# Optimization experiments

Hardware: AMD Instinct MI355X
Metric: run time of the kernel (lower is better)

The kernel has to match this reference:

```python
import jax, jax.numpy as jnp
import numpy as np

EMBED_DIM = 256
NUM_HEADS = 8
HEAD_WIDTH = 32
B, L = 2, 2048


def setup_inputs() -> dict:
    key = jax.random.key(0)
    k1, k2, k3, k4 = jax.random.split(key, 4)
    x = jax.random.normal(k1, (B, L, EMBED_DIM), dtype=jnp.float32)
    bias = jax.random.normal(k2, (B, L, L, NUM_HEADS), dtype=jnp.float32)
    # torch Linear weights: [out_features, in_features]
    W_proj = jax.random.normal(k3, (3 * EMBED_DIM, EMBED_DIM), dtype=jnp.float32) * (EMBED_DIM ** -0.5)
    W_o = jax.random.normal(k4, (EMBED_DIM, EMBED_DIM), dtype=jnp.float32) * (EMBED_DIM ** -0.5)
    b_o = jnp.zeros((EMBED_DIM,), dtype=jnp.float32)
    return {"x": x, "bias": bias, "W_proj": W_proj, "W_o": W_o, "b_o": b_o}


def reference(x, bias, W_proj, W_o, b_o):
    b, l, _ = x.shape
    h, hw = NUM_HEADS, HEAD_WIDTH
    # fused QKV projection: (b, l, 3*E)
    t = jnp.einsum('ble,fe->blf', x, W_proj)
    # rearrange '... l (h c) -> ... h l c' with c = 3*hw, then split
    t = t.reshape(b, l, h, 3 * hw).transpose(0, 2, 1, 3)  # (b, h, l, 3*hw)
    q, k, v = jnp.split(t, 3, axis=-1)
    q = q * (hw ** -0.5)
    a = jnp.einsum('bhqc,bhkc->bhqk', q, k)
    a = a + bias.transpose(0, 3, 1, 2)  # (b, h, lq, lk)
    a = jax.nn.softmax(a, axis=-1)
    y = jnp.einsum('bhqk,bhkc->bqhc', a, v)
    y = y.reshape(b, l, h * hw)
    return jnp.einsum('ble,fe->blf', y, W_o) + b_o
```

## Files before the change

### kernel.cpp

```cpp
#include <hip/hip_runtime.h>
#include <math.h>

#define NH   8
#define HW   32
#define LSEQ 2048
#define EMB  256
#define BB   2

typedef short bf16x8 __attribute__((ext_vector_type(8)));
typedef float f32x4  __attribute__((ext_vector_type(4)));
typedef unsigned short u16x4 __attribute__((ext_vector_type(4)));

__device__ __forceinline__ unsigned short f2bf(float x) {
  union { float f; unsigned u; } v; v.f = x;
  unsigned r = v.u + 0x7fffu + ((v.u >> 16) & 1u);
  return (unsigned short)(r >> 16);
}
__device__ __forceinline__ float bf2f(unsigned short h) {
  union { float f; unsigned u; } v; v.u = ((unsigned)h) << 16;
  return v.f;
}
__device__ __forceinline__ void split2(float x, unsigned short& h, unsigned short& l) {
  h = f2bf(x);
  l = f2bf(x - bf2f(h));
}

__global__ __launch_bounds__(256) void presplit(
    const float* __restrict__ X, const float* __restrict__ Wp,
    const float* __restrict__ Wo,
    unsigned short* __restrict__ Xh, unsigned short* __restrict__ Xl,
    unsigned short* __restrict__ Wph, unsigned short* __restrict__ Wpl,
    unsigned short* __restrict__ Woh, unsigned short* __restrict__ Wol) {
  const int NX = 4096 * 256, NP = 768 * 256, NO = 256 * 256;
  const int total4 = (NX + NP + NO) >> 2;
  int i4 = blockIdx.x * 256 + threadIdx.x;
  if (i4 >= total4) return;
  int e = i4 << 2;
  const float* src;
  unsigned short *dh, *dl;
  int off;
  if (e < NX)           { src = X;  dh = Xh;  dl = Xl;  off = e; }
  else if (e < NX + NP) { src = Wp; dh = Wph; dl = Wpl; off = e - NX; }
  else                  { src = Wo; dh = Woh; dl = Wol; off = e - NX - NP; }
  float4 v = *(const float4*)(src + off);
  u16x4 h, l;
  unsigned short hh, ll;
  split2(v.x, hh, ll); h[0] = hh; l[0] = ll;
  split2(v.y, hh, ll); h[1] = hh; l[1] = ll;
  split2(v.z, hh, ll); h[2] = hh; l[2] = ll;
  split2(v.w, hh, ll); h[3] = hh; l[3] = ll;
  *(u16x4*)(dh + off) = h;
  *(u16x4*)(dl + off) = l;
}

__global__ __launch_bounds__(256, 4) void qkv_gemm(
    const unsigned short* __restrict__ Xh, const unsigned short* __restrict__ Xl,
    const unsigned short* __restrict__ Wph, const unsigned short* __restrict__ Wpl,
    unsigned short* __restrict__ Qh, unsigned short* __restrict__ Ql,
    unsigned short* __restrict__ Kh, unsigned short* __restrict__ Kl,
    unsigned short* __restrict__ Vth, unsigned short* __restrict__ Vtl) {
  const int t = threadIdx.x;
  const int w = t >> 6, lane = t & 63;
  const int col = lane & 15, quad = lane >> 4;
  const int m0 = blockIdx.y * 64 + w * 16;
  const int n0 = blockIdx.x * 64;
  const size_t xoff = (size_t)(m0 + col) * 256 + quad * 8;

  f32x4 acc[4];
#pragma unroll
  for (int nt = 0; nt < 4; ++nt) acc[nt] = (f32x4){0.f, 0.f, 0.f, 0.f};

#pragma unroll
  for (int es = 0; es < 8; ++es) {
    bf16x8 ah = *(const bf16x8*)(Xh + xoff + es * 32);
    bf16x8 al = *(const bf16x8*)(Xl + xoff + es * 32);
#pragma unroll
    for (int nt = 0; nt < 4; ++nt) {
      const size_t woff = (size_t)(n0 + nt * 16 + col) * 256 + es * 32 + quad * 8;
      bf16x8 bh = *(const bf16x8*)(Wph + woff);
      bf16x8 bl = *(const bf16x8*)(Wpl + woff);
      acc[nt] = __builtin_amdgcn_mfma_f32_16x16x32_bf16(ah, bh, acc[nt], 0, 0, 0);
      acc[nt] = __builtin_amdgcn_mfma_f32_16x16x32_bf16(ah, bl, acc[nt], 0, 0, 0);
      acc[nt] = __builtin_amdgcn_mfma_f32_16x16x32_bf16(al, bh, acc[nt], 0, 0, 0);
    }
  }

  const float qscale = 0.17677669529663687f;
#pragma unroll
  for (int nt = 0; nt < 4; ++nt) {
    const int f = n0 + nt * 16 + col;
    const int hd = f / 96, r0 = f - hd * 96;
#pragma unroll
    for (int r = 0; r < 4; ++r) {
      const int m = m0 + quad * 4 + r;
      const int bbv = m >> 11, ll = m & 2047;
      float v = acc[nt][r];
      unsigned short hi, lo;
      if (r0 < 64) {
        float sv = (r0 < 32) ? v * qscale : v;
        split2(sv, hi, lo);
        size_t idx = ((size_t)(bbv * NH + hd) * LSEQ + ll) * HW + (r0 & 31);
        if (r0 < 32) { Qh[idx] = hi; Ql[idx] = lo; }
        else         { Kh[idx] = hi; Kl[idx] = lo; }
      } else {
        split2(v, hi, lo);
        size_t idx = ((size_t)(bbv * NH + hd) * HW + (r0 - 64)) * LSEQ + ll;
        Vth[idx] = hi; Vtl[idx] = lo;
      }
    }
  }
}

__global__ __launch_bounds__(512, 4) void attn(
    const unsigned short* __restrict__ Qh, const unsigned short* __restrict__ Ql,
    const unsigned short* __restrict__ Kh, const unsigned short* __restrict__ Kl,
    const unsigned short* __restrict__ Vth, const unsigned short* __restrict__ Vtl,
    const float* __restrict__ Bias, float* __restrict__ Yp,
    float* __restrict__ Mm, float* __restrict__ Ll) {
  __shared__ __attribute__((aligned(16))) float Bst[4 * 32 * 72];
  __shared__ __attribute__((aligned(16))) unsigned Pbuf[8 * 1152];
  const int t = threadIdx.x;
  const int w = t >> 6, lane = t & 63;
  const int col = lane & 15, quad = lane >> 4;
  const int head = w >> 1, wks = w & 1;
  const int x = blockIdx.x;
  const int p = ((x >> 4) << 3) | (x & 7);
  const int hh = (x >> 3) & 1;
  const int ks = p & 1;
  const int b = (p >> 1) & 1;
  const int q0g = (p >> 2) * 32;
  const int hg = hh * 4 + head;
  const int kbase = ks * 1024;

  const size_t bhoff = (size_t)(b * NH + hg) * LSEQ * HW;
  const unsigned short* Qhp = Qh + bhoff;
  const unsigned short* Qlp = Ql + bhoff;
  const unsigned short* Khp = Kh + bhoff;
  const unsigned short* Klp = Kl + bhoff;
  const unsigned short* Vhp = Vth + bhoff;
  const unsigned short* Vlp = Vtl + bhoff;
  unsigned* Pw = &Pbuf[w * 1152];

  bf16x8 Qbh[2], Qbl[2];
#pragma unroll
  for (int qt = 0; qt < 2; ++qt) {
    size_t off = (size_t)(q0g + qt * 16 + col) * HW + quad * 8;
    Qbh[qt] = *(const bf16x8*)(Qhp + off);
    Qbl[qt] = *(const bf16x8*)(Qlp + off);
  }

  f32x4 o[2][2];
#pragma unroll
  for (int ct = 0; ct < 2; ++ct)
#pragma unroll
    for (int qt = 0; qt < 2; ++qt) o[ct][qt] = (f32x4){0.f, 0.f, 0.f, 0.f};
  float m_i[2] = {-1e30f, -1e30f}, l_i[2] = {0.f, 0.f};

  const int sq = w, sk = lane;
  float4 bsr[4];
#pragma unroll
  for (int u = 0; u < 4; ++u)
    bsr[u] = *(const float4*)&Bias[(((size_t)(b * LSEQ + q0g + u * 8 + sq)) * LSEQ +
                                    kbase + sk) * NH + hh * 4];

#pragma unroll 1
  for (int it = 0; it < 16; ++it) {
    __syncthreads();
    const int kw = kbase + it * 64 + wks * 32;
    bf16x8 Kah[2], Kal[2], Vah[2], Val[2];
#pragma unroll
    for (int kt = 0; kt < 2; ++kt) {
      size_t off = (size_t)(kw + kt * 16 + col) * HW + quad * 8;
      Kah[kt] = *(const bf16x8*)(Khp + off);
      Kal[kt] = *(const bf16x8*)(Klp + off);
    }
#pragma unroll
    for (int ct = 0; ct < 2; ++ct) {
      size_t off = (size_t)(ct * 16 + col) * LSEQ + kw + quad * 8;
      Vah[ct] = *(const bf16x8*)(Vhp + off);
      Val[ct] = *(const bf16x8*)(Vlp + off);
    }
#pragma unroll
    for (int u = 0; u < 4; ++u) {
      const int qq = u * 8 + sq;
      Bst[0 * 2304 + qq * 72 + sk] = bsr[u].x;
      Bst[1 * 2304 + qq * 72 + sk] = bsr[u].y;
      Bst[2 * 2304 + qq * 72 + sk] = bsr[u].z;
      Bst[3 * 2304 + qq * 72 + sk] = bsr[u].w;
    }
    if (it < 15) {
#pragma unroll
      for (int u = 0; u < 4; ++u)
        bsr[u] = *(const float4*)&Bias[(((size_t)(b * LSEQ + q0g + u * 8 + sq)) * LSEQ +
                                        kbase + (it + 1) * 64 + sk) * NH + hh * 4];
    }
    __syncthreads();

    f32x4 s[2][2];
#pragma unroll
    for (int kt = 0; kt < 2; ++kt)
#pragma unroll
      for (int qt = 0; qt < 2; ++qt) {
        f32x4 a = *(const f32x4*)&Bst[head * 2304 + (qt * 16 + col) * 72 +
                                      wks * 32 + kt * 16 + quad * 4];
        a = __builtin_amdgcn_mfma_f32_16x16x32_bf16(Kah[kt], Qbh[qt], a, 0, 0, 0);
        a = __builtin_amdgcn_mfma_f32_16x16x32_bf16(Kah[kt], Qbl[qt], a, 0, 0, 0);
        a = __builtin_amdgcn_mfma_f32_16x16x32_bf16(Kal[kt], Qbh[qt], a, 0, 0, 0);
        s[kt][qt] = a;
      }

    float alpha[2];
#pragma unroll
    for (int qt = 0; qt < 2; ++qt) {
      float mx = s[0][qt][0];
#pragma unroll
      for (int r = 1; r < 4; ++r) mx = fmaxf(mx, s[0][qt][r]);
#pragma unroll
      for (int r = 0; r < 4; ++r) mx = fmaxf(mx, s[1][qt][r]);
      mx = fmaxf(mx, __shfl_xor(mx, 16, 64));
      mx = fmaxf(mx, __shfl_xor(mx, 32, 64));
      float mnew = fmaxf(m_i[qt], mx);
      float al = __expf(m_i[qt] - mnew);
      float ps = 0.f;
#pragma unroll
      for (int kt = 0; kt < 2; ++kt)
#pragma unroll
        for (int r = 0; r < 4; ++r) {
          float pv = __expf(s[kt][qt][r] - mnew);
          s[kt][qt][r] = pv;
          ps += pv;
        }
      ps += __shfl_xor(ps, 16, 64);
      ps += __shfl_xor(ps, 32, 64);
      l_i[qt] = l_i[qt] * al + ps;
      m_i[qt] = mnew;
      alpha[qt] = al;
#pragma unroll
      for (int ct = 0; ct < 2; ++ct)
#pragma unroll
        for (int r = 0; r < 4; ++r) o[ct][qt][r] *= al;
    }

#pragma unroll
    for (int kt = 0; kt < 2; ++kt)
#pragma unroll
      for (int qt = 0; qt < 2; ++qt)
#pragma unroll
        for (int r = 0; r < 4; ++r) {
          unsigned short hi, lo; split2(s[kt][qt][r], hi, lo);
          Pw[(kt * 16 + quad * 4 + r) * 34 + qt * 16 + col] =
              (unsigned)hi | ((unsigned)lo << 16);
        }
    bf16x8 Pbh[2], Pbl[2];
#pragma unroll
    for (int qt = 0; qt < 2; ++qt) {
#pragma unroll
      for (int j = 0; j < 8; ++j) {
        unsigned d = Pw[(quad * 8 + j) * 34 + qt * 16 + col];
        Pbh[qt][j] = (short)(d & 0xffffu);
        Pbl[qt][j] = (short)(d >> 16);
      }
    }
#pragma unroll
    for (int ct = 0; ct < 2; ++ct)
#pragma unroll
      for (int qt = 0; qt < 2; ++qt) {
        f32x4 a = o[ct][qt];
        a = __builtin_amdgcn_mfma_f32_16x16x32_bf16(Vah[ct], Pbh[qt], a, 0, 0, 0);
        a = __builtin_amdgcn_mfma_f32_16x16x32_bf16(Vah[ct], Pbl[qt], a, 0, 0, 0);
        a = __builtin_amdgcn_mfma_f32_16x16x32_bf16(Val[ct], Pbh[qt], a, 0, 0, 0);
        o[ct][qt] = a;
      }
  }

  __syncthreads();
  float* Pwf = (float*)Pw;
  if (wks == 1) {
#pragma unroll
    for (int ct = 0; ct < 2; ++ct)
#pragma unroll
      for (int qt = 0; qt < 2; ++qt)
#pragma unroll
        for (int r = 0; r < 4; ++r)
          Pwf[(ct * 16 + quad * 4 + r) * 34 + qt * 16 + col] = o[ct][qt][r];
    if (quad == 0) {
#pragma unroll
      for (int qt = 0; qt < 2; ++qt) {
        Pwf[1088 + qt * 16 + col] = m_i[qt];
        Pwf[1120 + qt * 16 + col] = l_i[qt];
      }
    }
  }
  __syncthreads();
  if (wks == 0) {
    const float* Pp = Pwf + 1152;
#pragma unroll
    for (int qt = 0; qt < 2; ++qt) {
      float m2 = Pp[1088 + qt * 16 + col];
      float l2 = Pp[1120 + qt * 16 + col];
      float mm = fmaxf(m_i[qt], m2);
      float a1 = __expf(m_i[qt] - mm);
      float a2 = __expf(m2 - mm);
      float lm = l_i[qt] * a1 + l2 * a2;
      const size_t row = (size_t)ks * 4096 + b * LSEQ + q0g + qt * 16 + col;
      if (quad == 0) {
        Mm[row * 8 + hg] = mm;
        Ll[row * 8 + hg] = lm;
      }
#pragma unroll
      for (int ct = 0; ct < 2; ++ct) {
        float4 res;
        res.x = o[ct][qt][0] * a1 + Pp[(ct * 16 + quad * 4 + 0) * 34 + qt * 16 + col] * a2;
        res.y = o[ct][qt][1] * a1 + Pp[(ct * 16 + quad * 4 + 1) * 34 + qt * 16 + col] * a2;
        res.z = o[ct][qt][2] * a1 + Pp[(ct * 16 + quad * 4 + 2) * 34 + qt * 16 + col] * a2;
        res.w = o[ct][qt][3] * a1 + Pp[(ct * 16 + quad * 4 + 3) * 34 + qt * 16 + col] * a2;
        *(float4*)&Yp[row * EMB + hg * HW + ct * 16 + quad * 4] = res;
      }
    }
  }
}

__global__ __launch_bounds__(256, 4) void out_gemm(
    const float* __restrict__ Yp, const float* __restrict__ Mm,
    const float* __restrict__ Ll, const unsigned short* __restrict__ Woh,
    const unsigned short* __restrict__ Wol, const float* __restrict__ bo,
    float* __restrict__ Out) {
  const int t = threadIdx.x;
  const int w = t >> 6, lane = t & 63;
  const int col = lane & 15, quad = lane >> 4;
  const int m0 = blockIdx.y * 64 + w * 16;
  const int n0 = blockIdx.x * 64;
  const int grow = m0 + col;
  const float* o1p = Yp + (size_t)grow * 256 + quad * 8;
  const float* o2p = o1p + (size_t)4096 * 256;

  float m1v[8], l1v[8], m2v[8], l2v[8];
  *(float4*)&m1v[0] = *(const float4*)&Mm[(size_t)grow * 8];
  *(float4*)&m1v[4] = *(const float4*)&Mm[(size_t)grow * 8 + 4];
  *(float4*)&l1v[0] = *(const float4*)&Ll[(size_t)grow * 8];
  *(float4*)&l1v[4] = *(const float4*)&Ll[(size_t)grow * 8 + 4];
  *(float4*)&m2v[0] = *(const float4*)&Mm[(size_t)(4096 + grow) * 8];
  *(float4*)&m2v[4] = *(const float4*)&Mm[(size_t)(4096 + grow) * 8 + 4];
  *(float4*)&l2v[0] = *(const float4*)&Ll[(size_t)(4096 + grow) * 8];
  *(float4*)&l2v[4] = *(const float4*)&Ll[(size_t)(4096 + grow) * 8 + 4];

  f32x4 acc[4];
#pragma unroll
  for (int nt = 0; nt < 4; ++nt) acc[nt] = (f32x4){0.f, 0.f, 0.f, 0.f};

#pragma unroll
  for (int es = 0; es < 8; ++es) {
    float M = fmaxf(m1v[es], m2v[es]);
    float w1 = __expf(m1v[es] - M), w2 = __expf(m2v[es] - M);
    float inv = 1.0f / (l1v[es] * w1 + l2v[es] * w2);
    w1 *= inv; w2 *= inv;
    float4 a1 = *(const float4*)(o1p + es * 32);
    float4 b1 = *(const float4*)(o1p + es * 32 + 4);
    float4 a2 = *(const float4*)(o2p + es * 32);
    float4 b2 = *(const float4*)(o2p + es * 32 + 4);
    float yv[8] = {a1.x * w1 + a2.x * w2, a1.y * w1 + a2.y * w2,
                   a1.z * w1 + a2.z * w2, a1.w * w1 + a2.w * w2,
                   b1.x * w1 + b2.x * w2, b1.y * w1 + b2.y * w2,
                   b1.z * w1 + b2.z * w2, b1.w * w1 + b2.w * w2};
    bf16x8 ah, al;
#pragma unroll
    for (int j = 0; j < 8; ++j) {
      unsigned short hi, lo; split2(yv[j], hi, lo);
      ah[j] = (short)hi; al[j] = (short)lo;
    }
#pragma unroll
    for (int nt = 0; nt < 4; ++nt) {
      const size_t woff = (size_t)(n0 + nt * 16 + col) * 256 + es * 32 + quad * 8;
      bf16x8 bh = *(const bf16x8*)(Woh + woff);
      bf16x8 bl = *(const bf16x8*)(Wol + woff);
      acc[nt] = __builtin_amdgcn_mfma_f32_16x16x32_bf16(ah, bh, acc[nt], 0, 0, 0);
      acc[nt] = __builtin_amdgcn_mfma_f32_16x16x32_bf16(ah, bl, acc[nt], 0, 0, 0);
      acc[nt] = __builtin_amdgcn_mfma_f32_16x16x32_bf16(al, bh, acc[nt], 0, 0, 0);
    }
  }
#pragma unroll
  for (int nt = 0; nt < 4; ++nt) {
    const int f = n0 + nt * 16 + col;
    const float bias_o = bo[f];
#pragma unroll
    for (int r = 0; r < 4; ++r)
      Out[(size_t)(m0 + quad * 4 + r) * 256 + f] = acc[nt][r] + bias_o;
  }
}

extern "C" void kernel_launch(void* const* d_in, const int* in_sizes, int n_in,
                              void* d_out, int out_size, void* d_ws, size_t ws_size,
                              hipStream_t stream) {
  const float* X    = (const float*)d_in[0];
  const float* Bias = (const float*)d_in[1];
  const float* Wp   = (const float*)d_in[2];
  const float* Wo   = (const float*)d_in[3];
  const float* bo   = (const float*)d_in[4];
  float* Out = (float*)d_out;

  const size_t qkv_elems = (size_t)BB * NH * LSEQ * HW;
  unsigned short* Qh  = (unsigned short*)d_ws;
  unsigned short* Ql  = Qh + qkv_elems;
  unsigned short* Kh  = Ql + qkv_elems;
  unsigned short* Kl  = Kh + qkv_elems;
  unsigned short* Vth = Kl + qkv_elems;
  unsigned short* Vtl = Vth + qkv_elems;
  float* Yp = (float*)(Vtl + qkv_elems);
  float* Mm = Yp + (size_t)2 * 4096 * 256;
  float* Ll = Mm + (size_t)2 * 4096 * 8;
  unsigned short* Xh  = (unsigned short*)(Ll + (size_t)2 * 4096 * 8);
  unsigned short* Xl  = Xh  + (size_t)4096 * 256;
  unsigned short* Wph = Xl  + (size_t)4096 * 256;
  unsigned short* Wpl = Wph + (size_t)768 * 256;
  unsigned short* Woh = Wpl + (size_t)768 * 256;
  unsigned short* Wol = Woh + (size_t)256 * 256;

  presplit<<<dim3(1280), 256, 0, stream>>>(X, Wp, Wo, Xh, Xl, Wph, Wpl, Woh, Wol);
  qkv_gemm<<<dim3(12, 64), 256, 0, stream>>>(Xh, Xl, Wph, Wpl, Qh, Ql, Kh, Kl, Vth, Vtl);
  attn<<<dim3(512), 512, 0, stream>>>(Qh, Ql, Kh, Kl, Vth, Vtl, Bias, Yp, Mm, Ll);
  out_gemm<<<dim3(4, 64), 256, 0, stream>>>(Yp, Mm, Ll, Woh, Wol, bo, Out);
}
```

Baseline: 448.8 us.

## Drop key-split in attention; use 16-query blocks over full keys, emit split bf16 Y

The attention kernel no longer splits the key range across two blocks with a later merge. Each block now handles 16 queries over all 2048 keys, so the grid stays at 512 blocks, and the final normalization happens inside the kernel. Attention writes Y directly as hi/lo bf16 pairs, so the output GEMM no longer reads two fp32 partials plus max/sum arrays or re-splits them. The cost is that each K/V tile is now reused by half as many queries, which doubles K/V load traffic per query, and the per-block loop is twice as long with smaller MFMA batches.

```diff
diff --git a/kernel.cpp b/kernel.cpp
--- a/kernel.cpp
+++ b/kernel.cpp
@@ -115,10 +115,10 @@
     const unsigned short* __restrict__ Qh, const unsigned short* __restrict__ Ql,
     const unsigned short* __restrict__ Kh, const unsigned short* __restrict__ Kl,
     const unsigned short* __restrict__ Vth, const unsigned short* __restrict__ Vtl,
-    const float* __restrict__ Bias, float* __restrict__ Yp,
-    float* __restrict__ Mm, float* __restrict__ Ll) {
-  __shared__ __attribute__((aligned(16))) float Bst[4 * 32 * 72];
-  __shared__ __attribute__((aligned(16))) unsigned Pbuf[8 * 1152];
+    const float* __restrict__ Bias,
+    unsigned short* __restrict__ Yh, unsigned short* __restrict__ Yl) {
+  __shared__ __attribute__((aligned(16))) float Bst[4 * 16 * 72];
+  __shared__ __attribute__((aligned(16))) unsigned Pbuf[8 * 576];
   const int t = threadIdx.x;
   const int w = t >> 6, lane = t & 63;
   const int col = lane & 15, quad = lane >> 4;
@@ -126,11 +126,9 @@
   const int x = blockIdx.x;
   const int p = ((x >> 4) << 3) | (x & 7);
   const int hh = (x >> 3) & 1;
-  const int ks = p & 1;
-  const int b = (p >> 1) & 1;
-  const int q0g = (p >> 2) * 32;
+  const int b = p & 1;
+  const int q0g = (p >> 1) * 16;
   const int hg = hh * 4 + head;
-  const int kbase = ks * 1024;
 
   const size_t bhoff = (size_t)(b * NH + hg) * LSEQ * HW;
   const unsigned short* Qhp = Qh + bhoff;
@@ -139,35 +137,32 @@
   const unsigned short* Klp = Kl + bhoff;
   const unsigned short* Vhp = Vth + bhoff;
   const unsigned short* Vlp = Vtl + bhoff;
-  unsigned* Pw = &Pbuf[w * 1152];
-
-  bf16x8 Qbh[2], Qbl[2];
-#pragma unroll
-  for (int qt = 0; qt < 2; ++qt) {
-    size_t off = (size_t)(q0g + qt * 16 + col) * HW + quad * 8;
-    Qbh[qt] = *(const bf16x8*)(Qhp + off);
-    Qbl[qt] = *(const bf16x8*)(Qlp + off);
-  }
-
-  f32x4 o[2][2];
-#pragma unroll
-  for (int ct = 0; ct < 2; ++ct)
-#pragma unroll
-    for (int qt = 0; qt < 2; ++qt) o[ct][qt] = (f32x4){0.f, 0.f, 0.f, 0.f};
-  float m_i[2] = {-1e30f, -1e30f}, l_i[2] = {0.f, 0.f};
+  unsigned* Pw = &Pbuf[w * 576];
+
+  bf16x8 Qbh, Qbl;
+  {
+    size_t off = (size_t)(q0g + col) * HW + quad * 8;
+    Qbh = *(const bf16x8*)(Qhp + off);
+    Qbl = *(const bf16x8*)(Qlp + off);
+  }
+
+  f32x4 o[2];
+#pragma unroll
+  for (int ct = 0; ct < 2; ++ct) o[ct] = (f32x4){0.f, 0.f, 0.f, 0.f};
+  float m_i = -1e30f, l_i = 0.f;
 
   const int sq = w, sk = lane;
-  float4 bsr[4];
-#pragma unroll
-  for (int u = 0; u < 4; ++u)
+  float4 bsr[2];
+#pragma unroll
+  for (int u = 0; u < 2; ++u)
     bsr[u] = *(const float4*)&Bias[(((size_t)(b * LSEQ + q0g + u * 8 + sq)) * LSEQ +
-                                    kbase + sk) * NH + hh * 4];
+                                    sk) * NH + hh * 4];
 
 #pragma unroll 1
-  for (int it = 0; it < 16; ++it) {
+  for (int it = 0; it < 32; ++it) {
     __syncthreads();
-    const int kw = kbase + it * 64 + wks * 32;
-    bf16x8 Kah[2], Kal[2], Vah[2], Val[2];
+    const int kw = it * 64 + wks * 32;
+    bf16x8 Kah[2], Kal[2];
 #pragma unroll
     for (int kt = 0; kt < 2; ++kt) {
       size_t off = (size_t)(kw + kt * 16 + col) * HW + quad * 8;
@@ -175,102 +170,92 @@
       Kal[kt] = *(const bf16x8*)(Klp + off);
     }
 #pragma unroll
+    for (int u = 0; u < 2; ++u) {
+      const int qq = u * 8 + sq;
+      Bst[0 * 1152 + qq * 72 + sk] = bsr[u].x;
+      Bst[1 * 1152 + qq * 72 + sk] = bsr[u].y;
+      Bst[2 * 1152 + qq * 72 + sk] = bsr[u].z;
+      Bst[3 * 1152 + qq * 72 + sk] = bsr[u].w;
+    }
+    if (it < 31) {
+#pragma unroll
+      for (int u = 0; u < 2; ++u)
+        bsr[u] = *(const float4*)&Bias[(((size_t)(b * LSEQ + q0g + u * 8 + sq)) * LSEQ +
+                                        (it + 1) * 64 + sk) * NH + hh * 4];
+    }
+    __syncthreads();
+
+    f32x4 s[2];
+#pragma unroll
+    for (int kt = 0; kt < 2; ++kt) {
+      f32x4 a = *(const f32x4*)&Bst[head * 1152 + col * 72 +
+                                    wks * 32 + kt * 16 + quad * 4];
+      a = __builtin_amdgcn_mfma_f32_16x16x32_bf16(Kah[kt], Qbh, a, 0, 0, 0);
+      a = __builtin_amdgcn_mfma_f32_16x16x32_bf16(Kah[kt], Qbl, a, 0, 0, 0);
+      a = __builtin_amdgcn_mfma_f32_16x16x32_bf16(Kal[kt], Qbh, a, 0, 0, 0);
+      s[kt] = a;
+    }
+
+    {
+      float mx = s[0][0];
+#pragma unroll
+      for (int r = 1; r < 4; ++r) mx = fmaxf(mx, s[0][r]);
+#pragma unroll
+      for (int r = 0; r < 4; ++r) mx = fmaxf(mx, s[1][r]);
+      mx = fmaxf(mx, __shfl_xor(mx, 16, 64));
+      mx = fmaxf(mx, __shfl_xor(mx, 32, 64));
+      float mnew = fmaxf(m_i, mx);
+      float al = __expf(m_i - mnew);
+      float ps = 0.f;
+#pragma unroll
+      for (int kt = 0; kt < 2; ++kt)
+#pragma unroll
+        for (int r = 0; r < 4; ++r) {
+          float pv = __expf(s[kt][r] - mnew);
+          s[kt][r] = pv;
+          ps += pv;
+        }
+      ps += __shfl_xor(ps, 16, 64);
+      ps += __shfl_xor(ps, 32, 64);
+      l_i = l_i * al + ps;
+      m_i = mnew;
+#pragma unroll
+      for (int ct = 0; ct < 2; ++ct)
+#pragma unroll
+        for (int r = 0; r < 4; ++r) o[ct][r] *= al;
+    }
+
+    bf16x8 Vah[2], Val[2];
+#pragma unroll
     for (int ct = 0; ct < 2; ++ct) {
       size_t off = (size_t)(ct * 16 + col) * LSEQ + kw + quad * 8;
       Vah[ct] = *(const bf16x8*)(Vhp + off);
       Val[ct] = *(const bf16x8*)(Vlp + off);
     }
-#pragma unroll
-    for (int u = 0; u < 4; ++u) {
-      const int qq = u * 8 + sq;
-      Bst[0 * 2304 + qq * 72 + sk] = bsr[u].x;
-      Bst[1 * 2304 + qq * 72 + sk] = bsr[u].y;
-      Bst[2 * 2304 + qq * 72 + sk] = bsr[u].z;
-      Bst[3 * 2304 + qq * 72 + sk] = bsr[u].w;
-    }
-    if (it < 15) {
-#pragma unroll
-      for (int u = 0; u < 4; ++u)
-        bsr[u] = *(const float4*)&Bias[(((size_t)(b * LSEQ + q0g + u * 8 + sq)) * LSEQ +
-                                        kbase + (it + 1) * 64 + sk) * NH + hh * 4];
-    }
-    __syncthreads();
-
-    f32x4 s[2][2];
+
 #pragma unroll
     for (int kt = 0; kt < 2; ++kt)
 #pragma unroll
-      for (int qt = 0; qt < 2; ++qt) {
-        f32x4 a = *(const f32x4*)&Bst[head * 2304 + (qt * 16 + col) * 72 +
-                                      wks * 32 + kt * 16 + quad * 4];
-        a = __builtin_amdgcn_mfma_f32_16x16x32_bf16(Kah[kt], Qbh[qt], a, 0, 0, 0);
-        a = __builtin_amdgcn_mfma_f32_16x16x32_bf16(Kah[kt], Qbl[qt], a, 0, 0, 0);
-        a = __builtin_amdgcn_mfma_f32_16x16x32_bf16(Kal[kt], Qbh[qt], a, 0, 0, 0);
-        s[kt][qt] = a;
+      for (int r = 0; r < 4; ++r) {
+        unsigned short hi, lo; split2(s[kt][r], hi, lo);
+        Pw[(kt * 16 + quad * 4 + r) * 17 + col] =
+            (unsigned)hi | ((unsigned)lo << 16);
       }
-
-    float alpha[2];
-#pragma unroll
-    for (int qt = 0; qt < 2; ++qt) {
-      float mx = s[0][qt][0];
-#pragma unroll
-      for (int r = 1; r < 4; ++r) mx = fmaxf(mx, s[0][qt][r]);
-#pragma unroll
-      for (int r = 0; r < 4; ++r) mx = fmaxf(mx, s[1][qt][r]);
-      mx = fmaxf(mx, __shfl_xor(mx, 16, 64));
-      mx = fmaxf(mx, __shfl_xor(mx, 32, 64));
-      float mnew = fmaxf(m_i[qt], mx);
-      float al = __expf(m_i[qt] - mnew);
-      float ps = 0.f;
-#pragma unroll
-      for (int kt = 0; kt < 2; ++kt)
-#pragma unroll
-        for (int r = 0; r < 4; ++r) {
-          float pv = __expf(s[kt][qt][r] - mnew);
-          s[kt][qt][r] = pv;
-          ps += pv;
-        }
-      ps += __shfl_xor(ps, 16, 64);
-      ps += __shfl_xor(ps, 32, 64);
-      l_i[qt] = l_i[qt] * al + ps;
-      m_i[qt] = mnew;
-      alpha[qt] = al;
-#pragma unroll
-      for (int ct = 0; ct < 2; ++ct)
-#pragma unroll
-        for (int r = 0; r < 4; ++r) o[ct][qt][r] *= al;
-    }
-
-#pragma unroll
-    for (int kt = 0; kt < 2; ++kt)
-#pragma unroll
-      for (int qt = 0; qt < 2; ++qt)
-#pragma unroll
-        for (int r = 0; r < 4; ++r) {
-          unsigned short hi, lo; split2(s[kt][qt][r], hi, lo);
-          Pw[(kt * 16 + quad * 4 + r) * 34 + qt * 16 + col] =
-              (unsigned)hi | ((unsigned)lo << 16);
-        }
-    bf16x8 Pbh[2], Pbl[2];
-#pragma unroll
-    for (int qt = 0; qt < 2; ++qt) {
-#pragma unroll
-      for (int j = 0; j < 8; ++j) {
-        unsigned d = Pw[(quad * 8 + j) * 34 + qt * 16 + col];
-        Pbh[qt][j] = (short)(d & 0xffffu);
-        Pbl[qt][j] = (short)(d >> 16);
-      }
-    }
-#pragma unroll
-    for (int ct = 0; ct < 2; ++ct)
-#pragma unroll
-      for (int qt = 0; qt < 2; ++qt) {
-        f32x4 a = o[ct][qt];
-        a = __builtin_amdgcn_mfma_f32_16x16x32_bf16(Vah[ct], Pbh[qt], a, 0, 0, 0);
-        a = __builtin_amdgcn_mfma_f32_16x16x32_bf16(Vah[ct], Pbl[qt], a, 0, 0, 0);
-        a = __builtin_amdgcn_mfma_f32_16x16x32_bf16(Val[ct], Pbh[qt], a, 0, 0, 0);
-        o[ct][qt] = a;
-      }
+    bf16x8 Pbh, Pbl;
+#pragma unroll
+    for (int j = 0; j < 8; ++j) {
+      unsigned d = Pw[(quad * 8 + j) * 17 + col];
+      Pbh[j] = (short)(d & 0xffffu);
+      Pbl[j] = (short)(d >> 16);
+    }
+#pragma unroll
+    for (int ct = 0; ct < 2; ++ct) {
+      f32x4 a = o[ct];
+      a = __builtin_amdgcn_mfma_f32_16x16x32_bf16(Vah[ct], Pbh, a, 0, 0, 0);
+      a = __builtin_amdgcn_mfma_f32_16x16x32_bf16(Vah[ct], Pbl, a, 0, 0, 0);
+      a = __builtin_amdgcn_mfma_f32_16x16x32_bf16(Val[ct], Pbh, a, 0, 0, 0);
+      o[ct] = a;
+    }
   }
 
   __syncthreads();
@@ -279,70 +264,50 @@
 #pragma unroll
     for (int ct = 0; ct < 2; ++ct)
 #pragma unroll
-      for (int qt = 0; qt < 2; ++qt)
-#pragma unroll
-        for (int r = 0; r < 4; ++r)
-          Pwf[(ct * 16 + quad * 4 + r) * 34 + qt * 16 + col] = o[ct][qt][r];
+      for (int r = 0; r < 4; ++r)
+        Pwf[(ct * 16 + quad * 4 + r) * 17 + col] = o[ct][r];
     if (quad == 0) {
-#pragma unroll
-      for (int qt = 0; qt < 2; ++qt) {
-        Pwf[1088 + qt * 16 + col] = m_i[qt];
-        Pwf[1120 + qt * 16 + col] = l_i[qt];
-      }
+      Pwf[544 + col] = m_i;
+      Pwf[560 + col] = l_i;
     }
   }
   __syncthreads();
   if (wks == 0) {
-    const float* Pp = Pwf + 1152;
-#pragma unroll
-    for (int qt = 0; qt < 2; ++qt) {
-      float m2 = Pp[1088 + qt * 16 + col];
-      float l2 = Pp[1120 + qt * 16 + col];
-      float mm = fmaxf(m_i[qt], m2);
-      float a1 = __expf(m_i[qt] - mm);
-      float a2 = __expf(m2 - mm);
-      float lm = l_i[qt] * a1 + l2 * a2;
-      const size_t row = (size_t)ks * 4096 + b * LSEQ + q0g + qt * 16 + col;
-      if (quad == 0) {
-        Mm[row * 8 + hg] = mm;
-        Ll[row * 8 + hg] = lm;
+    const float* Pp = Pwf + 576;
+    float m2 = Pp[544 + col];
+    float l2 = Pp[560 + col];
+    float mm = fmaxf(m_i, m2);
+    float a1 = __expf(m_i - mm);
+    float a2 = __expf(m2 - mm);
+    float inv = 1.0f / (l_i * a1 + l2 * a2);
+    a1 *= inv; a2 *= inv;
+    const size_t row = (size_t)(b * LSEQ + q0g + col);
+#pragma unroll
+    for (int ct = 0; ct < 2; ++ct) {
+      u16x4 rh, rl;
+#pragma unroll
+      for (int r = 0; r < 4; ++r) {
+        float res = o[ct][r] * a1 + Pp[(ct * 16 + quad * 4 + r) * 17 + col] * a2;
+        unsigned short hi, lo; split2(res, hi, lo);
+        rh[r] = hi; rl[r] = lo;
       }
-#pragma unroll
-      for (int ct = 0; ct < 2; ++ct) {
-        float4 res;
-        res.x = o[ct][qt][0] * a1 + Pp[(ct * 16 + quad * 4 + 0) * 34 + qt * 16 + col] * a2;
-        res.y = o[ct][qt][1] * a1 + Pp[(ct * 16 + quad * 4 + 1) * 34 + qt * 16 + col] * a2;
-        res.z = o[ct][qt][2] * a1 + Pp[(ct * 16 + quad * 4 + 2) * 34 + qt * 16 + col] * a2;
-        res.w = o[ct][qt][3] * a1 + Pp[(ct * 16 + quad * 4 + 3) * 34 + qt * 16 + col] * a2;
-        *(float4*)&Yp[row * EMB + hg * HW + ct * 16 + quad * 4] = res;
-      }
+      size_t idx = row * EMB + hg * HW + ct * 16 + quad * 4;
+      *(u16x4*)&Yh[idx] = rh;
+      *(u16x4*)&Yl[idx] = rl;
     }
   }
 }
 
 __global__ __launch_bounds__(256, 4) void out_gemm(
-    const float* __restrict__ Yp, const float* __restrict__ Mm,
-    const float* __restrict__ Ll, const unsigned short* __restrict__ Woh,
-    const unsigned short* __restrict__ Wol, const float* __restrict__ bo,
-    float* __restrict__ Out) {
+    const unsigned short* __restrict__ Yh, const unsigned short* __restrict__ Yl,
+    const unsigned short* __restrict__ Woh, const unsigned short* __restrict__ Wol,
+    const float* __restrict__ bo, float* __restrict__ Out) {
   const int t = threadIdx.x;
   const int w = t >> 6, lane = t & 63;
   const int col = lane & 15, quad = lane >> 4;
   const int m0 = blockIdx.y * 64 + w * 16;
   const int n0 = blockIdx.x * 64;
-  const int grow = m0 + col;
-  const float* o1p = Yp + (size_t)grow * 256 + quad * 8;
-  const float* o2p = o1p + (size_t)4096 * 256;
-
-  float m1v[8], l1v[8], m2v[8], l2v[8];
-  *(float4*)&m1v[0] = *(const float4*)&Mm[(size_t)grow * 8];
-  *(float4*)&m1v[4] = *(const float4*)&Mm[(size_t)grow * 8 + 4];
-  *(float4*)&l1v[0] = *(const float4*)&Ll[(size_t)grow * 8];
-  *(float4*)&l1v[4] = *(const float4*)&Ll[(size_t)grow * 8 + 4];
-  *(float4*)&m2v[0] = *(const float4*)&Mm[(size_t)(4096 + grow) * 8];
-  *(float4*)&m2v[4] = *(const float4*)&Mm[(size_t)(4096 + grow) * 8 + 4];
-  *(float4*)&l2v[0] = *(const float4*)&Ll[(size_t)(4096 + grow) * 8];
-  *(float4*)&l2v[4] = *(const float4*)&Ll[(size_t)(4096 + grow) * 8 + 4];
+  const size_t yoff = (size_t)(m0 + col) * 256 + quad * 8;
 
   f32x4 acc[4];
 #pragma unroll
@@ -350,24 +315,8 @@
 
 #pragma unroll
   for (int es = 0; es < 8; ++es) {
-    float M = fmaxf(m1v[es], m2v[es]);
-    float w1 = __expf(m1v[es] - M), w2 = __expf(m2v[es] - M);
-    float inv = 1.0f / (l1v[es] * w1 + l2v[es] * w2);
-    w1 *= inv; w2 *= inv;
-    float4 a1 = *(const float4*)(o1p + es * 32);
-    float4 b1 = *(const float4*)(o1p + es * 32 + 4);
-    float4 a2 = *(const float4*)(o2p + es * 32);
-    float4 b2 = *(const float4*)(o2p + es * 32 + 4);
-    float yv[8] = {a1.x * w1 + a2.x * w2, a1.y * w1 + a2.y * w2,
-                   a1.z * w1 + a2.z * w2, a1.w * w1 + a2.w * w2,
-                   b1.x * w1 + b2.x * w2, b1.y * w1 + b2.y * w2,
-                   b1.z * w1 + b2.z * w2, b1.w * w1 + b2.w * w2};
-    bf16x8 ah, al;
-#pragma unroll
-    for (int j = 0; j < 8; ++j) {
-      unsigned short hi, lo; split2(yv[j], hi, lo);
-      ah[j] = (short)hi; al[j] = (short)lo;
-    }
+    bf16x8 ah = *(const bf16x8*)(Yh + yoff + es * 32);
+    bf16x8 al = *(const bf16x8*)(Yl + yoff + es * 32);
 #pragma unroll
     for (int nt = 0; nt < 4; ++nt) {
       const size_t woff = (size_t)(n0 + nt * 16 + col) * 256 + es * 32 + quad * 8;
@@ -405,10 +354,9 @@
   unsigned short* Kl  = Kh + qkv_elems;
   unsigned short* Vth = Kl + qkv_elems;
   unsigned short* Vtl = Vth + qkv_elems;
-  float* Yp = (float*)(Vtl + qkv_elems);
-  float* Mm = Yp + (size_t)2 * 4096 * 256;
-  float* Ll = Mm + (size_t)2 * 4096 * 8;
-  unsigned short* Xh  = (unsigned short*)(Ll + (size_t)2 * 4096 * 8);
+  unsigned short* Yh  = Vtl + qkv_elems;
+  unsigned short* Yl  = Yh + (size_t)4096 * 256;
+  unsigned short* Xh  = Yl + (size_t)4096 * 256;
   unsigned short* Xl  = Xh  + (size_t)4096 * 256;
   unsigned short* Wph = Xl  + (size_t)4096 * 256;
   unsigned short* Wpl = Wph + (size_t)768 * 256;
@@ -417,6 +365,6 @@
 
   presplit<<<dim3(1280), 256, 0, stream>>>(X, Wp, Wo, Xh, Xl, Wph, Wpl, Woh, Wol);
   qkv_gemm<<<dim3(12, 64), 256, 0, stream>>>(Xh, Xl, Wph, Wpl, Qh, Ql, Kh, Kl, Vth, Vtl);
-  attn<<<dim3(512), 512, 0, stream>>>(Qh, Ql, Kh, Kl, Vth, Vtl, Bias, Yp, Mm, Ll);
-  out_gemm<<<dim3(4, 64), 256, 0, stream>>>(Yp, Mm, Ll, Woh, Wol, bo, Out);
-}
+  attn<<<dim3(512), 512, 0, stream>>>(Qh, Ql, Kh, Kl, Vth, Vtl, Bias, Yh, Yl);
+  out_gemm<<<dim3(4, 64), 256, 0, stream>>>(Yh, Yl, Woh, Wol, bo, Out);
+}
```

Measured after the change: 467.7 us. +4.2%, slower.
